# Optimization experiments

Measured on AMD Instinct MI355X. Metric: run time of the kernel, lower is better.

## Reference

```python
import jax, jax.numpy as jnp
import numpy as np

DIM = 768
HEADS = 12
HEAD_DIM = DIM // HEADS
SCALE = HEAD_DIM ** (-0.5)


def setup_inputs() -> dict:
    key = jax.random.key(0)
    k1, k2, k3 = jax.random.split(key, 3)
    x = jax.random.normal(k1, (4, 2048, DIM), dtype=jnp.float32)
    # nn.Linear(dim, 3*dim, bias=False): weight [3*dim, dim]
    w_qkv = jax.random.normal(k2, (3 * DIM, DIM), dtype=jnp.float32) * (DIM ** -0.5)
    # nn.Linear(dim, dim) with bias
    w_proj = jax.random.normal(k3, (DIM, DIM), dtype=jnp.float32) * (DIM ** -0.5)
    b_proj = jnp.zeros((DIM,), dtype=jnp.float32)
    return {"x": x, "w_qkv": w_qkv, "w_proj": w_proj, "b_proj": b_proj}


def reference(x, w_qkv, w_proj, b_proj):
    B, N, C = x.shape
    H, D = HEADS, HEAD_DIM
    qkv = jnp.einsum('bnc,oc->bno', x, w_qkv)  # [B,N,3C]
    qkv = qkv.reshape(B, N, 3, H, D).transpose(2, 0, 3, 1, 4)  # [3,B,H,N,D]
    q, k, v = qkv[0], qkv[1], qkv[2]
    attn = jnp.einsum('bhnd,bhmd->bhnm', q, k) * SCALE  # [B,H,N,N]
    attn = jax.nn.softmax(attn, axis=-1)
    attn = jax.nn.softmax(attn, axis=-1)  # double softmax, as in original
    out = jnp.einsum('bhnm,bhmd->bhnd', attn, v)  # [B,H,N,D]
    out = out.transpose(0, 2, 1, 3).reshape(B, N, C)
    return jnp.einsum('bnc,oc->bno', out, w_proj) + b_proj
```

## Files before the change

kernel.cpp:

```cpp
#include <hip/hip_runtime.h>
#include <hip/hip_bf16.h>

#define DIM 768
#define HEADS 12
#define HD 64
#define SEQ 2048
#define BATCH 4
#define BHN 48
#define TOK 8192

#if __has_builtin(__builtin_amdgcn_exp2f)
#define EXP2F __builtin_amdgcn_exp2f
#else
#define EXP2F exp2f
#endif
#define EXP_C 0.1803368801111244f

using short8  = __attribute__((ext_vector_type(8))) short;
using float4v = __attribute__((ext_vector_type(4))) float;

__device__ __forceinline__ short f2b(float f) {
    union { float f; unsigned u; } v; v.f = f;
    unsigned r = v.u + 0x7FFF + ((v.u >> 16) & 1);
    return (short)(r >> 16);
}
__device__ __forceinline__ float b2f(short s) {
    union { unsigned u; float f; } v;
    v.u = ((unsigned)(unsigned short)s) << 16;
    return v.f;
}
__device__ __forceinline__ unsigned pk2(float a, float b) {
    union { float f; unsigned u; } x, y; x.f = a; y.f = b;
    return ((x.u + 0x8000u) >> 16) | ((y.u + 0x8000u) & 0xFFFF0000u);
}

typedef const __attribute__((address_space(1))) unsigned GU;
typedef __attribute__((address_space(3))) unsigned LU;
__device__ __forceinline__ void gload_lds16(const short* g, short* l) {
    __builtin_amdgcn_global_load_lds((GU*)g, (LU*)l, 16, 0, 0);
}

__global__ void cast_all(const float* __restrict__ x, const float* __restrict__ wq,
                         const float* __restrict__ wp,
                         short* __restrict__ xb, short* __restrict__ wqb,
                         short* __restrict__ wpb, int nx4, int nq4) {
    int i = blockIdx.x * 256 + threadIdx.x;
    const float* in; short* out; int j = i;
    if (i < nx4)            { in = x;  out = xb;  }
    else if (i < nx4 + nq4) { in = wq; out = wqb; j = i - nx4; }
    else                    { in = wp; out = wpb; j = i - nx4 - nq4; }
    float4 f = ((const float4*)in)[j];
    short4 o;
    o.x = f2b(f.x); o.y = f2b(f.y); o.z = f2b(f.z); o.w = f2b(f.w);
    ((short4*)out)[j] = o;
}

__global__ void vsum_kernel(const short* __restrict__ Vw, float* __restrict__ Vsum) {
    int wid  = blockIdx.x * 4 + (threadIdx.x >> 6);
    int lane = threadIdx.x & 63;
    const short* row = Vw + (size_t)wid * SEQ;
    float s = 0.f;
    for (int i = lane; i < SEQ; i += 64) s += b2f(row[i]);
    #pragma unroll
    for (int m = 1; m < 64; m <<= 1) s += __shfl_xor(s, m, 64);
    if (lane == 0) Vsum[wid] = s;
}

__global__ __launch_bounds__(256, 4)
void gemm_qkv(const short* __restrict__ A, const short* __restrict__ Bw,
              short* __restrict__ Qw, short* __restrict__ Kw, short* __restrict__ Vw)
{
    __shared__ __align__(16) short As[2][128 * 32];
    __shared__ __align__(16) short Bs[2][128 * 32];

    const int tid  = threadIdx.x;
    const int lane = tid & 63;
    const int wave = tid >> 6;
    const int wm = (wave >> 1) * 64, wn = (wave & 1) * 64;
    const int l15 = lane & 15, quad = lane >> 4;

    const int gid = blockIdx.x;
    const int w   = gid >> 3;
    const int ybl = (gid & 7) * 8 + (w & 7);
    const int xbl = w >> 3;

    const bool vpart = (xbl >= 12);
    const short* rowsP = vpart ? (Bw + 1536 * 768) : A;
    const short* colsP = vpart ? A : Bw;
    const int m0 = vpart ? (xbl - 12) * 128 : ybl * 128;
    const int n0 = vpart ? ybl * 128 : xbl * 128;
    const int K = DIM;

    float4v acc[4][4];
    #pragma unroll
    for (int i = 0; i < 4; i++)
        #pragma unroll
        for (int j = 0; j < 4; j++)
            acc[i][j] = (float4v){0.f, 0.f, 0.f, 0.f};

    const int G0 = wave * 128 + lane;
    const int G1 = G0 + 64;
    const int rA0 = G0 >> 2, cA0 = (G0 & 3) * 8;
    const int rA1 = G1 >> 2, cA1 = (G1 & 3) * 8;
    const int ldsoff = wave * 1024;

    for (int kt = 0; kt < K; kt += 64) {
        #pragma unroll
        for (int s = 0; s < 2; s++) {
            const int kc = kt + s * 32;
            gload_lds16(&rowsP[(size_t)(m0 + rA0) * K + kc + cA0], &As[s][ldsoff]);
            gload_lds16(&rowsP[(size_t)(m0 + rA1) * K + kc + cA1], &As[s][ldsoff + 512]);
            gload_lds16(&colsP[(size_t)(n0 + rA0) * K + kc + cA0], &Bs[s][ldsoff]);
            gload_lds16(&colsP[(size_t)(n0 + rA1) * K + kc + cA1], &Bs[s][ldsoff + 512]);
        }
        __syncthreads();
        #pragma unroll
        for (int s = 0; s < 2; s++) {
            short8 af[4], bfr[4];
            #pragma unroll
            for (int t = 0; t < 4; t++) {
                af[t]  = *(const short8*)&As[s][(wm + t * 16 + l15) * 32 + quad * 8];
                bfr[t] = *(const short8*)&Bs[s][(wn + t * 16 + l15) * 32 + quad * 8];
            }
            #pragma unroll
            for (int tm = 0; tm < 4; tm++)
                #pragma unroll
                for (int tn = 0; tn < 4; tn++)
                    acc[tm][tn] = __builtin_amdgcn_mfma_f32_16x16x32_bf16(af[tm], bfr[tn], acc[tm][tn], 0, 0, 0);
        }
        __syncthreads();
    }

    #pragma unroll
    for (int tm = 0; tm < 4; tm++)
        #pragma unroll
        for (int tn = 0; tn < 4; tn++)
            #pragma unroll
            for (int r = 0; r < 4; r++) {
                int row = m0 + wm + tm * 16 + quad * 4 + r;
                int col = n0 + wn + tn * 16 + l15;
                float v = acc[tm][tn][r];
                if (vpart) {
                    int hh = row >> 6, d = row & 63;
                    int b = col >> 11, n = col & 2047;
                    Vw[((size_t)(b * HEADS + hh) * 64 + d) * SEQ + n] = f2b(v);
                } else {
                    int hh = (col & 767) >> 6, d = col & 63;
                    int b = row >> 11, n = row & 2047;
                    int bh = b * HEADS + hh;
                    if (col < 768) Qw[((size_t)bh * SEQ + n) * 64 + d] = f2b(v * EXP_C);
                    else           Kw[((size_t)bh * SEQ + n) * 64 + d] = f2b(v);
                }
            }
}

__global__ __launch_bounds__(256, 4)
void gemm_proj(const short* __restrict__ A, const short* __restrict__ Bw,
               const float* __restrict__ bias, float* __restrict__ Out)
{
    __shared__ __align__(16) short As[2][128 * 32];
    __shared__ __align__(16) short Bs[2][64 * 32];

    const int tid  = threadIdx.x;
    const int lane = tid & 63;
    const int wave = tid >> 6;
    const int wm = (wave >> 1) * 64, wn = (wave & 1) * 32;
    const int l15 = lane & 15, quad = lane >> 4;

    const int gid = blockIdx.x;
    const int w   = gid >> 3;
    const int ybl = (gid & 7) * 8 + (w & 7);
    const int xbl = w >> 3;
    const int m0 = ybl * 128, n0 = xbl * 64;
    const int K = DIM;

    float4v acc[4][2];
    #pragma unroll
    for (int i = 0; i < 4; i++)
        #pragma unroll
        for (int j = 0; j < 2; j++)
            acc[i][j] = (float4v){0.f, 0.f, 0.f, 0.f};

    const int GA0 = wave * 128 + lane, GA1 = GA0 + 64;
    const int rA0 = GA0 >> 2, cA0 = (GA0 & 3) * 8;
    const int rA1 = GA1 >> 2, cA1 = (GA1 & 3) * 8;
    const int GB0 = wave * 64 + lane;
    const int rB0 = GB0 >> 2, cB0 = (GB0 & 3) * 8;
    const int ldsoffA = wave * 1024, ldsoffB = wave * 512;

    for (int kt = 0; kt < K; kt += 64) {
        #pragma unroll
        for (int s = 0; s < 2; s++) {
            const int kc = kt + s * 32;
            gload_lds16(&A [(size_t)(m0 + rA0) * K + kc + cA0], &As[s][ldsoffA]);
            gload_lds16(&A [(size_t)(m0 + rA1) * K + kc + cA1], &As[s][ldsoffA + 512]);
            gload_lds16(&Bw[(size_t)(n0 + rB0) * K + kc + cB0], &Bs[s][ldsoffB]);
        }
        __syncthreads();
        #pragma unroll
        for (int s = 0; s < 2; s++) {
            short8 af[4], bfr[2];
            #pragma unroll
            for (int t = 0; t < 4; t++)
                af[t] = *(const short8*)&As[s][(wm + t * 16 + l15) * 32 + quad * 8];
            #pragma unroll
            for (int t = 0; t < 2; t++)
                bfr[t] = *(const short8*)&Bs[s][(wn + t * 16 + l15) * 32 + quad * 8];
            #pragma unroll
            for (int tm = 0; tm < 4; tm++)
                #pragma unroll
                for (int tn = 0; tn < 2; tn++)
                    acc[tm][tn] = __builtin_amdgcn_mfma_f32_16x16x32_bf16(af[tm], bfr[tn], acc[tm][tn], 0, 0, 0);
        }
        __syncthreads();
    }

    #pragma unroll
    for (int tm = 0; tm < 4; tm++)
        #pragma unroll
        for (int tn = 0; tn < 2; tn++)
            #pragma unroll
            for (int r = 0; r < 4; r++) {
                int row = m0 + wm + tm * 16 + quad * 4 + r;
                int col = n0 + wn + tn * 16 + l15;
                Out[(size_t)row * 768 + col] = acc[tm][tn][r] + bias[col];
            }
}

__global__ __launch_bounds__(256, 3)
void attn_kernel(const short* __restrict__ Qw, const short* __restrict__ Kw,
                 const short* __restrict__ Vw, const float* __restrict__ Vsum,
                 short* __restrict__ Ow)
{
    __shared__ __align__(16) short KE[128 * 72];
    __shared__ __align__(16) short Eb[64 * 136];
    __shared__ __align__(16) short Vt[64 * 136];

    const int tid  = threadIdx.x;
    const int lane = tid & 63, wave = tid >> 6;
    const int l15 = lane & 15, quad = lane >> 4;
    const int bh = blockIdx.x >> 5;
    const int n0 = (blockIdx.x & 31) * 64;
    const int wq = (wave & 2) * 16;
    const int wk = (wave & 1) * 64;

    const short* Qp = Qw + (size_t)bh * SEQ * 64;
    const short* Kp = Kw + (size_t)bh * SEQ * 64;
    const short* Vp = Vw + (size_t)bh * 64 * SEQ;

    short8 onesf;
    #pragma unroll
    for (int j = 0; j < 8; j++) onesf[j] = (l15 == 0) ? (short)0x3F80 : (short)0;

    #pragma unroll
    for (int h = 0; h < 2; h++) {
        int c = tid + h * 256;
        int row = c >> 3, cc = (c & 7) * 8;
        *(short8*)&Eb[row * 72 + cc] = *(const short8*)&Qp[(size_t)(n0 + row) * 64 + cc];
    }
    __syncthreads();
    short8 aq[2][2];
    #pragma unroll
    for (int nb = 0; nb < 2; nb++)
        #pragma unroll
        for (int kk = 0; kk < 2; kk++)
            aq[nb][kk] = *(const short8*)&Eb[(wq + nb * 16 + l15) * 72 + kk * 32 + quad * 8];

    float4v Aacc[2][4], Lacc[2];
    #pragma unroll
    for (int mb = 0; mb < 2; mb++) {
        Lacc[mb] = (float4v){0.f, 0.f, 0.f, 0.f};
        #pragma unroll
        for (int t = 0; t < 4; t++) Aacc[mb][t] = (float4v){0.f, 0.f, 0.f, 0.f};
    }

    short8 kr[4], vr[4];
    #pragma unroll
    for (int h = 0; h < 4; h++) {
        int c = tid + h * 256;
        int row = c >> 3, cc = (c & 7) * 8;
        kr[h] = *(const short8*)&Kp[(size_t)row * 64 + cc];
        int vrow = c >> 4, vc = (c & 15) * 8;
        vr[h] = *(const short8*)&Vp[(size_t)vrow * SEQ + vc];
    }

    for (int kt = 0; kt < 16; kt++) {
        __syncthreads();
        #pragma unroll
        for (int h = 0; h < 4; h++) {
            int c = tid + h * 256;
            int row = c >> 3, cc = (c & 7) * 8;
            *(short8*)&KE[row * 72 + cc] = kr[h];
            int vrow = c >> 4, vc = (c & 15) * 8;
            *(short8*)&Vt[vrow * 136 + vc] = vr[h];
        }
        __syncthreads();

        if (kt < 15) {
            #pragma unroll
            for (int h = 0; h < 4; h++) {
                int c = tid + h * 256;
                int row = c >> 3, cc = (c & 7) * 8;
                kr[h] = *(const short8*)&Kp[(size_t)((kt + 1) * 128 + row) * 64 + cc];
                int vrow = c >> 4, vc = (c & 15) * 8;
                vr[h] = *(const short8*)&Vp[(size_t)vrow * SEQ + (kt + 1) * 128 + vc];
            }
        }

        float4v sacc[2][4];
        #pragma unroll
        for (int nb = 0; nb < 2; nb++)
            #pragma unroll
            for (int tn = 0; tn < 4; tn++) sacc[nb][tn] = (float4v){0.f, 0.f, 0.f, 0.f};
        #pragma unroll
        for (int tn = 0; tn < 4; tn++) {
            const int rowK = (wk + tn * 16 + l15) * 72;
            short8 b0 = *(const short8*)&KE[rowK + quad * 8];
            short8 b1 = *(const short8*)&KE[rowK + 32 + quad * 8];
            #pragma unroll
            for (int nb = 0; nb < 2; nb++) {
                sacc[nb][tn] = __builtin_amdgcn_mfma_f32_16x16x32_bf16(b0, aq[nb][0], sacc[nb][tn], 0, 0, 0);
                sacc[nb][tn] = __builtin_amdgcn_mfma_f32_16x16x32_bf16(b1, aq[nb][1], sacc[nb][tn], 0, 0, 0);
            }
        }

        #pragma unroll
        for (int nb = 0; nb < 2; nb++) {
            const int qrow = (wq + nb * 16 + l15) * 136;
            #pragma unroll
            for (int tn = 0; tn < 4; tn++) {
                float e0 = EXP2F(sacc[nb][tn][0]);
                float e1 = EXP2F(sacc[nb][tn][1]);
                float e2 = EXP2F(sacc[nb][tn][2]);
                float e3 = EXP2F(sacc[nb][tn][3]);
                uint2 u; u.x = pk2(e0, e1); u.y = pk2(e2, e3);
                *(uint2*)&Eb[qrow + wk + tn * 16 + quad * 4] = u;
            }
        }

        #pragma unroll
        for (int ks = 0; ks < 2; ks++) {
            const int koff = wk + ks * 32 + quad * 8;
            short8 ae0 = *(const short8*)&Eb[(wq + l15) * 136 + koff];
            short8 ae1 = *(const short8*)&Eb[(wq + 16 + l15) * 136 + koff];
            Lacc[0] = __builtin_amdgcn_mfma_f32_16x16x32_bf16(ae0, onesf, Lacc[0], 0, 0, 0);
            Lacc[1] = __builtin_amdgcn_mfma_f32_16x16x32_bf16(ae1, onesf, Lacc[1], 0, 0, 0);
            #pragma unroll
            for (int tn = 0; tn < 4; tn++) {
                short8 bv = *(const short8*)&Vt[(tn * 16 + l15) * 136 + koff];
                Aacc[0][tn] = __builtin_amdgcn_mfma_f32_16x16x32_bf16(ae0, bv, Aacc[0][tn], 0, 0, 0);
                Aacc[1][tn] = __builtin_amdgcn_mfma_f32_16x16x32_bf16(ae1, bv, Aacc[1][tn], 0, 0, 0);
            }
        }
    }

    __syncthreads();
    float* KEf = (float*)KE;
    float* Vtf = (float*)Vt;
    const int p = wave >> 1;
    if (wave & 1) {
        #pragma unroll
        for (int mb = 0; mb < 2; mb++) {
            #pragma unroll
            for (int tn = 0; tn < 4; tn++)
                #pragma unroll
                for (int r = 0; r < 4; r++)
                    KEf[(mb * 16 + tn * 4 + r) * 128 + p * 64 + lane] = Aacc[mb][tn][r];
            #pragma unroll
            for (int r = 0; r < 4; r++)
                Vtf[(mb * 4 + r) * 128 + p * 64 + lane] = Lacc[mb][r];
        }
    }
    __syncthreads();
    if (!(wave & 1)) {
        float il[2][4];
        #pragma unroll
        for (int mb = 0; mb < 2; mb++)
            #pragma unroll
            for (int r = 0; r < 4; r++) {
                float ls = Lacc[mb][r] + Vtf[(mb * 4 + r) * 128 + p * 64 + lane];
                il[mb][r] = 1.f / __shfl(ls, lane & 48, 64);
            }
        const int b = bh / HEADS, hh = bh - (bh / HEADS) * HEADS;
        #pragma unroll
        for (int tn = 0; tn < 4; tn++) {
            int d = tn * 16 + l15;
            float vs = Vsum[bh * 64 + d];
            #pragma unroll
            for (int mb = 0; mb < 2; mb++)
                #pragma unroll
                for (int r = 0; r < 4; r++) {
                    float a = Aacc[mb][tn][r] + KEf[(mb * 16 + tn * 4 + r) * 128 + p * 64 + lane];
                    int row = n0 + wq + mb * 16 + quad * 4 + r;
                    float val = (vs + a * il[mb][r]) * (1.f / 2049.f);
                    int tok = b * SEQ + row;
                    Ow[(size_t)tok * 768 + hh * 64 + d] = f2b(val);
                }
        }
    }
}

extern "C" void kernel_launch(void* const* d_in, const int* in_sizes, int n_in,
                              void* d_out, int out_size, void* d_ws, size_t ws_size,
                              hipStream_t stream) {
    const float* x      = (const float*)d_in[0];
    const float* w_qkv  = (const float*)d_in[1];
    const float* w_proj = (const float*)d_in[2];
    const float* b_proj = (const float*)d_in[3];
    float* out = (float*)d_out;

    char* ws = (char*)d_ws;
    size_t off = 0;
    auto alloc = [&](size_t bytes) {
        void* p = ws + off;
        off += (bytes + 255) & ~(size_t)255;
        return p;
    };
    short* x_bf  = (short*)alloc((size_t)TOK * DIM * 2);
    short* wq_bf = (short*)alloc((size_t)3 * DIM * DIM * 2);
    short* wp_bf = (short*)alloc((size_t)DIM * DIM * 2);
    short* Qw    = (short*)alloc((size_t)BHN * SEQ * 64 * 2);
    short* Kw    = (short*)alloc((size_t)BHN * SEQ * 64 * 2);
    short* Vw    = (short*)alloc((size_t)BHN * SEQ * 64 * 2);
    short* Ow    = (short*)alloc((size_t)TOK * DIM * 2);
    float* Vsum  = (float*)alloc((size_t)BHN * 64 * 4);

    int nx4 = TOK * DIM / 4, nq4 = 3 * DIM * DIM / 4, np4 = DIM * DIM / 4;
    int tot4 = nx4 + nq4 + np4;
    cast_all<<<tot4 / 256, 256, 0, stream>>>(x, w_qkv, w_proj, x_bf, wq_bf, wp_bf, nx4, nq4);

    gemm_qkv<<<1152, 256, 0, stream>>>(x_bf, wq_bf, Qw, Kw, Vw);

    vsum_kernel<<<BHN * 64 / 4, 256, 0, stream>>>(Vw, Vsum);

    attn_kernel<<<BHN * 32, 256, 0, stream>>>(Qw, Kw, Vw, Vsum, Ow);

    gemm_proj<<<768, 256, 0, stream>>>(Ow, wp_bf, b_proj, out);
}
```

Measured before the change: 227.8 us.

## Keep exp scores in registers and feed PV via 16x16x16 MFMA, dropping LDS round-trip

The attention kernel no longer writes exponentiated scores to a shared-memory buffer and reads them back. The QK^T MFMA output layout is reused directly as the A operand of 16x16x16 bf16 MFMAs for the row-sum and PV products. This removes the Eb buffer and its LDS traffic, and the lower shared-memory use lets launch bounds rise to 4 blocks per CU. In exchange it issues twice as many smaller MFMAs with narrower V loads, and register pressure under the tighter bound could cause spills.

```diff
diff --git a/kernel.cpp b/kernel.cpp
--- a/kernel.cpp
+++ b/kernel.cpp
@@ -17,6 +17,7 @@
 #define EXP_C 0.1803368801111244f
 
 using short8  = __attribute__((ext_vector_type(8))) short;
+using short4v = __attribute__((ext_vector_type(4))) short;
 using float4v = __attribute__((ext_vector_type(4))) float;
 
 __device__ __forceinline__ short f2b(float f) {
@@ -227,13 +228,12 @@
             }
 }
 
-__global__ __launch_bounds__(256, 3)
+__global__ __launch_bounds__(256, 4)
 void attn_kernel(const short* __restrict__ Qw, const short* __restrict__ Kw,
                  const short* __restrict__ Vw, const float* __restrict__ Vsum,
                  short* __restrict__ Ow)
 {
     __shared__ __align__(16) short KE[128 * 72];
-    __shared__ __align__(16) short Eb[64 * 136];
     __shared__ __align__(16) short Vt[64 * 136];
 
     const int tid  = threadIdx.x;
@@ -248,15 +248,15 @@
     const short* Kp = Kw + (size_t)bh * SEQ * 64;
     const short* Vp = Vw + (size_t)bh * 64 * SEQ;
 
-    short8 onesf;
-    #pragma unroll
-    for (int j = 0; j < 8; j++) onesf[j] = (l15 == 0) ? (short)0x3F80 : (short)0;
+    short4v ones4;
+    #pragma unroll
+    for (int j = 0; j < 4; j++) ones4[j] = (l15 == 0) ? (short)0x3F80 : (short)0;
 
     #pragma unroll
     for (int h = 0; h < 2; h++) {
         int c = tid + h * 256;
         int row = c >> 3, cc = (c & 7) * 8;
-        *(short8*)&Eb[row * 72 + cc] = *(const short8*)&Qp[(size_t)(n0 + row) * 64 + cc];
+        *(short8*)&KE[row * 72 + cc] = *(const short8*)&Qp[(size_t)(n0 + row) * 64 + cc];
     }
     __syncthreads();
     short8 aq[2][2];
@@ -264,7 +264,7 @@
     for (int nb = 0; nb < 2; nb++)
         #pragma unroll
         for (int kk = 0; kk < 2; kk++)
-            aq[nb][kk] = *(const short8*)&Eb[(wq + nb * 16 + l15) * 72 + kk * 32 + quad * 8];
+            aq[nb][kk] = *(const short8*)&KE[(wq + nb * 16 + l15) * 72 + kk * 32 + quad * 8];
 
     float4v Aacc[2][4], Lacc[2];
     #pragma unroll
@@ -307,11 +307,7 @@
             }
         }
 
-        float4v sacc[2][4];
-        #pragma unroll
-        for (int nb = 0; nb < 2; nb++)
-            #pragma unroll
-            for (int tn = 0; tn < 4; tn++) sacc[nb][tn] = (float4v){0.f, 0.f, 0.f, 0.f};
+        short4v ae16[2][4];
         #pragma unroll
         for (int tn = 0; tn < 4; tn++) {
             const int rowK = (wk + tn * 16 + l15) * 72;
@@ -319,37 +315,29 @@
             short8 b1 = *(const short8*)&KE[rowK + 32 + quad * 8];
             #pragma unroll
             for (int nb = 0; nb < 2; nb++) {
-                sacc[nb][tn] = __builtin_amdgcn_mfma_f32_16x16x32_bf16(b0, aq[nb][0], sacc[nb][tn], 0, 0, 0);
-                sacc[nb][tn] = __builtin_amdgcn_mfma_f32_16x16x32_bf16(b1, aq[nb][1], sacc[nb][tn], 0, 0, 0);
-            }
-        }
-
-        #pragma unroll
-        for (int nb = 0; nb < 2; nb++) {
-            const int qrow = (wq + nb * 16 + l15) * 136;
+                float4v s = (float4v){0.f, 0.f, 0.f, 0.f};
+                s = __builtin_amdgcn_mfma_f32_16x16x32_bf16(b0, aq[nb][0], s, 0, 0, 0);
+                s = __builtin_amdgcn_mfma_f32_16x16x32_bf16(b1, aq[nb][1], s, 0, 0, 0);
+                float e0 = EXP2F(s[0]);
+                float e1 = EXP2F(s[1]);
+                float e2 = EXP2F(s[2]);
+                float e3 = EXP2F(s[3]);
+                union { short4v s4; uint2 u; } pe;
+                pe.u.x = pk2(e0, e1);
+                pe.u.y = pk2(e2, e3);
+                ae16[nb][tn] = pe.s4;
+            }
+        }
+
+        #pragma unroll
+        for (int tk = 0; tk < 4; tk++) {
+            Lacc[0] = __builtin_amdgcn_mfma_f32_16x16x16bf16_1k(ae16[0][tk], ones4, Lacc[0], 0, 0, 0);
+            Lacc[1] = __builtin_amdgcn_mfma_f32_16x16x16bf16_1k(ae16[1][tk], ones4, Lacc[1], 0, 0, 0);
             #pragma unroll
             for (int tn = 0; tn < 4; tn++) {
-                float e0 = EXP2F(sacc[nb][tn][0]);
-                float e1 = EXP2F(sacc[nb][tn][1]);
-                float e2 = EXP2F(sacc[nb][tn][2]);
-                float e3 = EXP2F(sacc[nb][tn][3]);
-                uint2 u; u.x = pk2(e0, e1); u.y = pk2(e2, e3);
-                *(uint2*)&Eb[qrow + wk + tn * 16 + quad * 4] = u;
-            }
-        }
-
-        #pragma unroll
-        for (int ks = 0; ks < 2; ks++) {
-            const int koff = wk + ks * 32 + quad * 8;
-            short8 ae0 = *(const short8*)&Eb[(wq + l15) * 136 + koff];
-            short8 ae1 = *(const short8*)&Eb[(wq + 16 + l15) * 136 + koff];
-            Lacc[0] = __builtin_amdgcn_mfma_f32_16x16x32_bf16(ae0, onesf, Lacc[0], 0, 0, 0);
-            Lacc[1] = __builtin_amdgcn_mfma_f32_16x16x32_bf16(ae1, onesf, Lacc[1], 0, 0, 0);
-            #pragma unroll
-            for (int tn = 0; tn < 4; tn++) {
-                short8 bv = *(const short8*)&Vt[(tn * 16 + l15) * 136 + koff];
-                Aacc[0][tn] = __builtin_amdgcn_mfma_f32_16x16x32_bf16(ae0, bv, Aacc[0][tn], 0, 0, 0);
-                Aacc[1][tn] = __builtin_amdgcn_mfma_f32_16x16x32_bf16(ae1, bv, Aacc[1][tn], 0, 0, 0);
+                short4v bv = *(const short4v*)&Vt[(tn * 16 + l15) * 136 + wk + tk * 16 + quad * 4];
+                Aacc[0][tn] = __builtin_amdgcn_mfma_f32_16x16x16bf16_1k(ae16[0][tk], bv, Aacc[0][tn], 0, 0, 0);
+                Aacc[1][tn] = __builtin_amdgcn_mfma_f32_16x16x16bf16_1k(ae16[1][tk], bv, Aacc[1][tn], 0, 0, 0);
             }
         }
     }
```

Result: no change. 229.6 us (+0.8%).
